# Performance work log

Hardware: AMD Instinct MI355X
Metric: run time of the kernel (lower is better)

Reference implementation:

```python
import jax, jax.numpy as jnp
import numpy as np

N_USERS = 50000
N_ITEMS = 50000
N = N_USERS + N_ITEMS
DIM = 64
N_LAYERS = 3
N_EDGES = 1250000
BN_EPS = 1e-5


def setup_inputs() -> dict:
    key = jax.random.key(0)
    k_x, k_e, k_w, k_b = jax.random.split(key, 4)
    x = jax.random.normal(k_x, (N, DIM), dtype=jnp.float32)
    edge_index = jax.random.randint(k_e, (2, N_EDGES), 0, N, dtype=jnp.int64)
    # Glorot-ish init for the per-layer GCNConv linear weights [L, DIM, DIM]
    Ws = jax.random.normal(k_w, (N_LAYERS, DIM, DIM), dtype=jnp.float32) * (1.0 / np.sqrt(DIM))
    bs = jnp.zeros((N_LAYERS, DIM), dtype=jnp.float32)
    gamma = jnp.ones((DIM,), dtype=jnp.float32)
    beta = jnp.zeros((DIM,), dtype=jnp.float32)
    return {"x": x, "edge_index": edge_index, "Ws": Ws, "bs": bs,
            "gamma": gamma, "beta": beta}


def _gcn_conv(x, W, b, src, dst, deg_inv_sqrt):
    # PyG GCNConv: h = x @ W^T ; out_i = sum_{j->i} norm_ji * h_j + b
    h = x @ W.T                                   # [N, DIM]
    norm = deg_inv_sqrt[src] * deg_inv_sqrt[dst]  # [E2]
    msg = h[src] * norm[:, None]                  # gather over irregular edges
    out = jax.ops.segment_sum(msg, dst, num_segments=N)
    return out + b


def reference(x, edge_index, Ws, bs, gamma, beta):
    # Add self-loops once (same augmented graph for every layer).
    loops = jnp.arange(N, dtype=edge_index.dtype)
    src = jnp.concatenate([edge_index[0], loops])  # source nodes j
    dst = jnp.concatenate([edge_index[1], loops])  # target nodes i
    # Symmetric normalization degrees (edge weight 1, counted at targets).
    deg = jax.ops.segment_sum(jnp.ones_like(dst, dtype=x.dtype), dst, num_segments=N)
    deg_inv_sqrt = jnp.where(deg > 0, jax.lax.rsqrt(deg), 0.0)

    for i in range(N_LAYERS):
        x = _gcn_conv(x, Ws[i], bs[i], src, dst, deg_inv_sqrt)

    # BatchNorm1d (training-mode batch statistics, biased variance)
    mean = jnp.mean(x, axis=0)
    var = jnp.mean((x - mean) ** 2, axis=0)
    x = (x - mean) * jax.lax.rsqrt(var + BN_EPS) * gamma + beta

    users, items = x[:N_USERS], x[N_USERS:]
    return users, items
```

## Files before the change

kernel.cpp:

```cpp
#include <hip/hip_runtime.h>

#define NN      100000
#define NUSERS  50000
#define NE      1250000
#define DIM     64
#define BN_EPS  1e-5f
#define NBUCK   8
#define NCHUNK  320
#define SLOT    40

typedef __attribute__((ext_vector_type(8))) short s16x8;
typedef __attribute__((ext_vector_type(4))) float f32x4;

__device__ __forceinline__ short f2b(float f) {
    unsigned u = __builtin_bit_cast(unsigned, f);
    u = (u + 0x7fffu + ((u >> 16) & 1u)) >> 16;
    return (short)u;
}
__device__ __forceinline__ float b2f(unsigned short s) {
    unsigned u = ((unsigned)s) << 16;
    return __builtin_bit_cast(float, u);
}

__global__ __launch_bounds__(256) void place_part(const int* __restrict__ ei,
                                                  int* __restrict__ cursor,
                                                  int* __restrict__ csr_src) {
    __shared__ int Qd[4][128];
    __shared__ int Qs[4][128];
    int lane = threadIdx.x & 63, wave = threadIdx.x >> 6;
    int B = blockIdx.x & (NBUCK - 1);
    int gw = (blockIdx.x >> 3) * 4 + wave;
    const int NW  = NCHUNK * 4;
    const int per = (NE + NW - 1) / NW;
    int e0 = gw * per;
    int e1 = e0 + per; if (e1 > NE) e1 = NE;
    int qn = 0;
    for (int e = e0 + lane; e - lane < e1; e += 64) {
        bool keep = false; int d = 0, s = 0;
        if (e < e1) {
            d = __builtin_nontemporal_load(&ei[NE + e]);
            keep = ((d / 12500) == B);
            if (keep) s = __builtin_nontemporal_load(&ei[e]);
        }
        unsigned long long m = __ballot(keep);
        if (keep) {
            int rank = __popcll(m & ((1ull << lane) - 1ull));
            Qd[wave][qn + rank] = d;
            Qs[wave][qn + rank] = s;
        }
        qn += __popcll(m);
        if (qn >= 64) {
            int dd = Qd[wave][lane];
            int ss = Qs[wave][lane];
            int pos = atomicAdd(&cursor[dd], 1);
            if (pos < SLOT) csr_src[dd * SLOT + pos] = ss;
            qn -= 64;
            int mvd = (lane < qn) ? Qd[wave][64 + lane] : 0;
            int mvs = (lane < qn) ? Qs[wave][64 + lane] : 0;
            if (lane < qn) { Qd[wave][lane] = mvd; Qs[wave][lane] = mvs; }
        }
    }
    if (lane < qn) {
        int dd = Qd[wave][lane];
        int pos = atomicAdd(&cursor[dd], 1);
        if (pos < SLOT) csr_src[dd * SLOT + pos] = Qs[wave][lane];
    }
}

__global__ __launch_bounds__(256) void dinv_kernel(const int* __restrict__ cursor,
                                                   float* __restrict__ dinv) {
    int v = blockIdx.x * blockDim.x + threadIdx.x;
    if (v < NN) dinv[v] = rsqrtf((float)cursor[v] + 1.0f);
}

__global__ __launch_bounds__(128) void c0_kernel(const float* __restrict__ Ws,
                                                 const float* __restrict__ bs,
                                                 float* __restrict__ c0) {
    int t = threadIdx.x;
    if (t < 128) {
        int l = t >> 6, j = t & 63;
        const float* Wl = Ws + (size_t)(l + 1) * 4096;
        const float* bl = bs + l * 64;
        float s = 0.0f;
        for (int k = 0; k < 64; ++k) s += bl[k] * Wl[j * 64 + k];
        c0[t] = s;
    }
}

template <int L0>
__global__ __launch_bounds__(256) void gemm_mfma(const void* __restrict__ Xin,
                                                 const float* __restrict__ W,
                                                 const float* __restrict__ dinv,
                                                 const float* __restrict__ c0,
                                                 unsigned short* __restrict__ Gb) {
    int lane = threadIdx.x & 63;
    int n16 = lane & 15, quad = lane >> 4;

    s16x8 bfrag[4][2];
#pragma unroll
    for (int t = 0; t < 4; ++t)
#pragma unroll
        for (int c = 0; c < 2; ++c) {
            const float4* wp = (const float4*)(W + (t * 16 + n16) * 64 + c * 32 + quad * 8);
            float4 w0 = wp[0], w1 = wp[1];
            s16x8 f;
            f[0] = f2b(w0.x); f[1] = f2b(w0.y); f[2] = f2b(w0.z); f[3] = f2b(w0.w);
            f[4] = f2b(w1.x); f[5] = f2b(w1.y); f[6] = f2b(w1.z); f[7] = f2b(w1.w);
            bfrag[t][c] = f;
        }

    int wid = (blockIdx.x * blockDim.x + threadIdx.x) >> 6;
    int nw  = (gridDim.x * blockDim.x) >> 6;
    for (int tile = wid; tile < NN / 16; tile += nw) {
        int r0 = tile * 16;
        int m  = r0 + n16;
        s16x8 a[2];
#pragma unroll
        for (int c = 0; c < 2; ++c) {
            if (L0) {
                const float4* xp = (const float4*)((const float*)Xin + (size_t)m * 64 + c * 32 + quad * 8);
                float4 x0 = xp[0], x1 = xp[1];
                s16x8 f;
                f[0] = f2b(x0.x); f[1] = f2b(x0.y); f[2] = f2b(x0.z); f[3] = f2b(x0.w);
                f[4] = f2b(x1.x); f[5] = f2b(x1.y); f[6] = f2b(x1.z); f[7] = f2b(x1.w);
                a[c] = f;
            } else {
                a[c] = *(const s16x8*)((const unsigned short*)Xin + (size_t)m * 64 + c * 32 + quad * 8);
            }
        }
        f32x4 acc[4] = {{0,0,0,0},{0,0,0,0},{0,0,0,0},{0,0,0,0}};
#pragma unroll
        for (int c = 0; c < 2; ++c)
#pragma unroll
            for (int t = 0; t < 4; ++t)
                acc[t] = __builtin_amdgcn_mfma_f32_16x16x32_bf16(a[c], bfrag[t][c], acc[t], 0, 0, 0);

        float dvr[4];
#pragma unroll
        for (int r = 0; r < 4; ++r) dvr[r] = dinv[r0 + quad * 4 + r];
#pragma unroll
        for (int t = 0; t < 4; ++t) {
            float cc = L0 ? 0.0f : c0[t * 16 + n16];
#pragma unroll
            for (int r = 0; r < 4; ++r) {
                float dv = dvr[r];
                float g  = L0 ? dv * acc[t][r] : dv * dv * acc[t][r] + dv * cc;
                Gb[(size_t)(r0 + quad * 4 + r) * 64 + t * 16 + n16] = (unsigned short)f2b(g);
            }
        }
    }
}

__global__ __launch_bounds__(256) void gather_b(const int* __restrict__ cursor,
                                                const int* __restrict__ csr_src,
                                                const unsigned short* __restrict__ Gb,
                                                unsigned short* __restrict__ ACCb) {
    int lane = threadIdx.x & 63;
    int c = lane & 15, g = lane >> 4;
    int wid  = (blockIdx.x * blockDim.x + threadIdx.x) >> 6;
    int nw   = (gridDim.x * blockDim.x) >> 6;
    for (int v = wid * 2; v < NN; v += nw * 2) {
        int w = v + 1;
        int n0 = cursor[v]; if (n0 > SLOT) n0 = SLOT;
        int n1 = cursor[w]; if (n1 > SLOT) n1 = SLOT;
        float m0 = (g == 0) ? 1.0f : 0.0f;
        float a0x, a0y, a0z, a0w, a1x, a1y, a1z, a1w;
        {
            ushort4 s0 = *(const ushort4*)(Gb + (size_t)v * 64 + c * 4);
            ushort4 s1 = *(const ushort4*)(Gb + (size_t)w * 64 + c * 4);
            a0x = m0 * b2f(s0.x); a0y = m0 * b2f(s0.y);
            a0z = m0 * b2f(s0.z); a0w = m0 * b2f(s0.w);
            a1x = m0 * b2f(s1.x); a1y = m0 * b2f(s1.y);
            a1z = m0 * b2f(s1.z); a1w = m0 * b2f(s1.w);
        }
        int idx0 = (lane < n0) ? csr_src[v * SLOT + lane] : 0;
        int idx1 = (lane < n1) ? csr_src[w * SLOT + lane] : 0;
        int nmax = (n0 > n1) ? n0 : n1;
        for (int t = 0; t < nmax; t += 16) {
            ushort4 val0[4], val1[4];
            float msk0[4], msk1[4];
#pragma unroll
            for (int u = 0; u < 4; ++u) {
                int nb = t + u * 4 + g;
                int s0 = __shfl(idx0, nb & 63, 64);
                int s1 = __shfl(idx1, nb & 63, 64);
                bool ok0 = nb < n0, ok1 = nb < n1;
                msk0[u] = ok0 ? 1.0f : 0.0f;
                msk1[u] = ok1 ? 1.0f : 0.0f;
                val0[u] = *(const ushort4*)(Gb + (size_t)(ok0 ? s0 : v) * 64 + c * 4);
                val1[u] = *(const ushort4*)(Gb + (size_t)(ok1 ? s1 : w) * 64 + c * 4);
            }
#pragma unroll
            for (int u = 0; u < 4; ++u) {
                a0x = fmaf(msk0[u], b2f(val0[u].x), a0x);
                a0y = fmaf(msk0[u], b2f(val0[u].y), a0y);
                a0z = fmaf(msk0[u], b2f(val0[u].z), a0z);
                a0w = fmaf(msk0[u], b2f(val0[u].w), a0w);
                a1x = fmaf(msk1[u], b2f(val1[u].x), a1x);
                a1y = fmaf(msk1[u], b2f(val1[u].y), a1y);
                a1z = fmaf(msk1[u], b2f(val1[u].z), a1z);
                a1w = fmaf(msk1[u], b2f(val1[u].w), a1w);
            }
        }
#pragma unroll
        for (int off = 16; off < 64; off <<= 1) {
            a0x += __shfl_xor(a0x, off, 64); a0y += __shfl_xor(a0y, off, 64);
            a0z += __shfl_xor(a0z, off, 64); a0w += __shfl_xor(a0w, off, 64);
            a1x += __shfl_xor(a1x, off, 64); a1y += __shfl_xor(a1y, off, 64);
            a1z += __shfl_xor(a1z, off, 64); a1w += __shfl_xor(a1w, off, 64);
        }
        if (g == 0) {
            ushort4 o0, o1;
            o0.x = (unsigned short)f2b(a0x); o0.y = (unsigned short)f2b(a0y);
            o0.z = (unsigned short)f2b(a0z); o0.w = (unsigned short)f2b(a0w);
            o1.x = (unsigned short)f2b(a1x); o1.y = (unsigned short)f2b(a1y);
            o1.z = (unsigned short)f2b(a1z); o1.w = (unsigned short)f2b(a1w);
            *(ushort4*)(ACCb + (size_t)v * 64 + c * 4) = o0;
            *(ushort4*)(ACCb + (size_t)w * 64 + c * 4) = o1;
        }
    }
}

__global__ __launch_bounds__(256) void bn_stats(const unsigned short* __restrict__ ACCb,
                                                const float* __restrict__ dinv,
                                                const float* __restrict__ blast,
                                                float* __restrict__ sums) {
    int j = threadIdx.x & 63;
    float b = blast[j];
    int wid = (blockIdx.x * blockDim.x + threadIdx.x) >> 6;
    int nw  = (gridDim.x * blockDim.x) >> 6;
    float s = 0.0f, s2 = 0.0f;
    for (int v = wid; v < NN; v += nw) {
        float y = dinv[v] * b2f(ACCb[(size_t)v * 64 + j]) + b;
        s += y;
        s2 += y * y;
    }
    __shared__ float ls[256], ls2[256];
    ls[threadIdx.x] = s;
    ls2[threadIdx.x] = s2;
    __syncthreads();
    if (threadIdx.x < 64) {
        s  = ls[threadIdx.x] + ls[threadIdx.x + 64] + ls[threadIdx.x + 128] + ls[threadIdx.x + 192];
        s2 = ls2[threadIdx.x] + ls2[threadIdx.x + 64] + ls2[threadIdx.x + 128] + ls2[threadIdx.x + 192];
        atomicAdd(&sums[j], s);
        atomicAdd(&sums[64 + j], s2);
    }
}

__global__ __launch_bounds__(256) void bn_apply(const unsigned short* __restrict__ ACCb,
                                                const float* __restrict__ dinv,
                                                const float* __restrict__ blast,
                                                const float* __restrict__ sums,
                                                const float* __restrict__ gamma,
                                                const float* __restrict__ beta,
                                                float* __restrict__ out) {
    const float invN = 1.0f / (float)NN;
    int stride = gridDim.x * blockDim.x;
    for (int i = blockIdx.x * blockDim.x + threadIdx.x; i < NN * 64; i += stride) {
        int j = i & 63;
        int v = i >> 6;
        float mean = sums[j] * invN;
        float var  = sums[64 + j] * invN - mean * mean;
        float y = dinv[v] * b2f(ACCb[i]) + blast[j];
        out[i] = (y - mean) * rsqrtf(var + BN_EPS) * gamma[j] + beta[j];
    }
}

extern "C" void kernel_launch(void* const* d_in, const int* in_sizes, int n_in,
                              void* d_out, int out_size, void* d_ws, size_t ws_size,
                              hipStream_t stream) {
    const float* x     = (const float*)d_in[0];
    const int*   ei    = (const int*)d_in[1];
    const float* Ws    = (const float*)d_in[2];
    const float* bs    = (const float*)d_in[3];
    const float* gamma = (const float*)d_in[4];
    const float* beta  = (const float*)d_in[5];
    float* out = (float*)d_out;

    char* ws = (char*)d_ws;
    size_t off = 0;
    unsigned short* ACCb = (unsigned short*)(ws + off); off += (size_t)NN * 64 * 2;
    unsigned short* Gb   = (unsigned short*)(ws + off); off += (size_t)NN * 64 * 2;
    float* dinv    = (float*)(ws + off); off += (size_t)NN * 4;
    float* sums    = (float*)(ws + off); off += 128 * 4;
    float* c0      = (float*)(ws + off); off += 128 * 4;
    int*   cursor  = (int*)(ws + off);   off += (size_t)NN * 4;
    int*   csr_src = (int*)(ws + off);   off += (size_t)NN * SLOT * 4;

    hipMemsetAsync(cursor, 0, NN * sizeof(int), stream);
    hipMemsetAsync(sums, 0, 128 * sizeof(float), stream);

    place_part<<<NBUCK * NCHUNK, 256, 0, stream>>>(ei, cursor, csr_src);
    dinv_kernel<<<(NN + 255) / 256, 256, 0, stream>>>(cursor, dinv);
    c0_kernel<<<1, 128, 0, stream>>>(Ws, bs, c0);

    gemm_mfma<1><<<1563, 256, 0, stream>>>(x, Ws, dinv, nullptr, Gb);
    gather_b<<<3072, 256, 0, stream>>>(cursor, csr_src, Gb, ACCb);
    for (int l = 1; l < 3; ++l) {
        gemm_mfma<0><<<1563, 256, 0, stream>>>(ACCb, Ws + (size_t)l * 4096, dinv,
                                               c0 + (l - 1) * 64, Gb);
        gather_b<<<3072, 256, 0, stream>>>(cursor, csr_src, Gb, ACCb);
    }

    bn_stats<<<2048, 256, 0, stream>>>(ACCb, dinv, bs + 128, sums);
    bn_apply<<<2048, 256, 0, stream>>>(ACCb, dinv, bs + 128, sums, gamma, beta, out);
}
```

Baseline: 382.9 us.

## Pad per-node cursors and simplify edge placement with unrolled direct atomics

Edge placement drops the LDS ballot/compaction queue and instead has each lane load 8 edges unrolled and issue its own atomicAdd on the destination cursor. The cursor array is padded to one counter per 32 bytes so concurrent atomics on neighbouring nodes do not share a cache line. Bucket-to-chunk assignment is rotated so buckets start on different edge ranges, and the chunk count drops. In exchange, source indices are now loaded for every edge rather than only kept ones, and the memset and cursor footprint grow eightfold.

```diff
diff --git a/kernel.cpp b/kernel.cpp
--- a/kernel.cpp
+++ b/kernel.cpp
@@ -6,8 +6,9 @@
 #define DIM     64
 #define BN_EPS  1e-5f
 #define NBUCK   8
-#define NCHUNK  320
+#define NCHUNK  256
 #define SLOT    40
+#define CPAD    8
 
 typedef __attribute__((ext_vector_type(8))) short s16x8;
 typedef __attribute__((ext_vector_type(4))) float f32x4;
@@ -25,52 +26,41 @@
 __global__ __launch_bounds__(256) void place_part(const int* __restrict__ ei,
                                                   int* __restrict__ cursor,
                                                   int* __restrict__ csr_src) {
-    __shared__ int Qd[4][128];
-    __shared__ int Qs[4][128];
     int lane = threadIdx.x & 63, wave = threadIdx.x >> 6;
     int B = blockIdx.x & (NBUCK - 1);
     int gw = (blockIdx.x >> 3) * 4 + wave;
-    const int NW  = NCHUNK * 4;
+    const int NW = NCHUNK * 4;
+    int gwr = gw + B * (NW / NBUCK);
+    if (gwr >= NW) gwr -= NW;
     const int per = (NE + NW - 1) / NW;
-    int e0 = gw * per;
+    int e0 = gwr * per;
     int e1 = e0 + per; if (e1 > NE) e1 = NE;
-    int qn = 0;
-    for (int e = e0 + lane; e - lane < e1; e += 64) {
-        bool keep = false; int d = 0, s = 0;
-        if (e < e1) {
-            d = __builtin_nontemporal_load(&ei[NE + e]);
-            keep = ((d / 12500) == B);
-            if (keep) s = __builtin_nontemporal_load(&ei[e]);
-        }
-        unsigned long long m = __ballot(keep);
-        if (keep) {
-            int rank = __popcll(m & ((1ull << lane) - 1ull));
-            Qd[wave][qn + rank] = d;
-            Qs[wave][qn + rank] = s;
-        }
-        qn += __popcll(m);
-        if (qn >= 64) {
-            int dd = Qd[wave][lane];
-            int ss = Qs[wave][lane];
-            int pos = atomicAdd(&cursor[dd], 1);
-            if (pos < SLOT) csr_src[dd * SLOT + pos] = ss;
-            qn -= 64;
-            int mvd = (lane < qn) ? Qd[wave][64 + lane] : 0;
-            int mvs = (lane < qn) ? Qs[wave][64 + lane] : 0;
-            if (lane < qn) { Qd[wave][lane] = mvd; Qs[wave][lane] = mvs; }
-        }
-    }
-    if (lane < qn) {
-        int dd = Qd[wave][lane];
-        int pos = atomicAdd(&cursor[dd], 1);
-        if (pos < SLOT) csr_src[dd * SLOT + pos] = Qs[wave][lane];
+    for (int eb = e0; eb < e1; eb += 8 * 64) {
+        int d[8], s[8];
+        bool k[8];
+#pragma unroll
+        for (int u = 0; u < 8; ++u) {
+            int ee = eb + u * 64 + lane;
+            bool in = ee < e1;
+            int idx = in ? ee : e0;
+            d[u] = ei[NE + idx];
+            s[u] = ei[idx];
+            k[u] = in && ((d[u] / 12500) == B);
+        }
+#pragma unroll
+        for (int u = 0; u < 8; ++u) {
+            if (k[u]) {
+                int pos = atomicAdd(&cursor[d[u] * CPAD], 1);
+                if (pos < SLOT) csr_src[d[u] * SLOT + pos] = s[u];
+            }
+        }
     }
 }
 
 __global__ __launch_bounds__(256) void dinv_kernel(const int* __restrict__ cursor,
                                                    float* __restrict__ dinv) {
     int v = blockIdx.x * blockDim.x + threadIdx.x;
-    if (v < NN) dinv[v] = rsqrtf((float)cursor[v] + 1.0f);
+    if (v < NN) dinv[v] = rsqrtf((float)cursor[v * CPAD] + 1.0f);
 }
 
 __global__ __launch_bounds__(128) void c0_kernel(const float* __restrict__ Ws,
@@ -161,8 +151,8 @@
     int nw   = (gridDim.x * blockDim.x) >> 6;
     for (int v = wid * 2; v < NN; v += nw * 2) {
         int w = v + 1;
-        int n0 = cursor[v]; if (n0 > SLOT) n0 = SLOT;
-        int n1 = cursor[w]; if (n1 > SLOT) n1 = SLOT;
+        int n0 = cursor[v * CPAD]; if (n0 > SLOT) n0 = SLOT;
+        int n1 = cursor[w * CPAD]; if (n1 > SLOT) n1 = SLOT;
         float m0 = (g == 0) ? 1.0f : 0.0f;
         float a0x, a0y, a0z, a0w, a1x, a1y, a1z, a1w;
         {
@@ -284,10 +274,10 @@
     float* dinv    = (float*)(ws + off); off += (size_t)NN * 4;
     float* sums    = (float*)(ws + off); off += 128 * 4;
     float* c0      = (float*)(ws + off); off += 128 * 4;
-    int*   cursor  = (int*)(ws + off);   off += (size_t)NN * 4;
+    int*   cursor  = (int*)(ws + off);   off += (size_t)NN * CPAD * 4;
     int*   csr_src = (int*)(ws + off);   off += (size_t)NN * SLOT * 4;
 
-    hipMemsetAsync(cursor, 0, NN * sizeof(int), stream);
+    hipMemsetAsync(cursor, 0, (size_t)NN * CPAD * sizeof(int), stream);
     hipMemsetAsync(sums, 0, 128 * sizeof(float), stream);
 
     place_part<<<NBUCK * NCHUNK, 256, 0, stream>>>(ei, cursor, csr_src);
```

New measurement: 361.5 us. 5.6% less time.
